# Performance work log

Measured on AMD Instinct MI355X. Metric: run time of the kernel, lower is better.

Reference implementation:

```python
import jax, jax.numpy as jnp
import numpy as np

D_MODEL = 512
D_FFN = 4 * D_MODEL
EPS = 1e-5


def layer_norm(x, gamma, beta):
    mu = jnp.mean(x, axis=-1, keepdims=True)
    var = jnp.mean(jnp.square(x - mu), axis=-1, keepdims=True)
    return (x - mu) * jax.lax.rsqrt(var + EPS) * gamma + beta


def setup_inputs() -> dict:
    key = jax.random.key(0)
    ks = jax.random.split(key, 12)
    B, S, D, F = 4, 2048, D_MODEL, D_FFN
    s = 1.0 / np.sqrt(D)
    inp = {
        "q": jax.random.normal(ks[0], (B, S, D), jnp.float32),
        "k": jax.random.normal(ks[1], (B, S, D), jnp.float32),
        "v": jax.random.normal(ks[2], (B, S, D), jnp.float32),
        "x": jax.random.normal(ks[3], (B, S, D), jnp.float32),
        "Wq": jax.random.normal(ks[4], (D, D), jnp.float32) * s,
        "bq": jnp.zeros((D,), jnp.float32),
        "Wk": jax.random.normal(ks[5], (D, D), jnp.float32) * s,
        "bk": jnp.zeros((D,), jnp.float32),
        "Wv": jax.random.normal(ks[6], (D, D), jnp.float32) * s,
        "bv": jnp.zeros((D,), jnp.float32),
        "g1": jnp.ones((D,), jnp.float32),
        "be1": jnp.zeros((D,), jnp.float32),
        "W1": jax.random.normal(ks[7], (D, F), jnp.float32) * s,
        "b1": jnp.zeros((F,), jnp.float32),
        "W2": jax.random.normal(ks[8], (F, D), jnp.float32) * (1.0 / np.sqrt(F)),
        "b2": jnp.zeros((D,), jnp.float32),
        "g2": jnp.ones((D,), jnp.float32),
        "be2": jnp.zeros((D,), jnp.float32),
    }
    return inp


def reference(q, k, v, x, Wq, bq, Wk, bk, Wv, bv, g1, be1, W1, b1, W2, b2, g2, be2):
    # QKV projections: [B,S,D] @ [D,D]
    Q = jnp.einsum("bsd,de->bse", q, Wq) + bq
    K = jnp.einsum("bsd,de->bse", k, Wk) + bk
    V = jnp.einsum("bsd,de->bse", v, Wv) + bv
    d_k = Q.shape[-1]
    # scaled dot-product attention, full [B,S,S] scores as in the original
    scores = jnp.einsum("bqd,bkd->bqk", Q, K) / jnp.sqrt(jnp.float32(d_k))
    probs = jax.nn.softmax(scores, axis=-1)
    attn = jnp.einsum("bqk,bkd->bqd", probs, V)
    # residual + LayerNorm
    h = layer_norm(attn + x, g1, be1)
    # position-wise FFN
    f = jnp.maximum(jnp.einsum("bsd,df->bsf", h, W1) + b1, 0.0)
    f = jnp.einsum("bsf,fd->bsd", f, W2) + b2
    # residual + LayerNorm
    return layer_norm(f + h, g2, be2)
```

## Files before the change

### kernel.cpp

```cpp
#include <hip/hip_runtime.h>


typedef __attribute__((ext_vector_type(8))) short short8;
typedef __attribute__((ext_vector_type(4))) float f32x4;

__device__ __forceinline__ unsigned short f2bf(float f) {
    unsigned int u = __float_as_uint(f);
    unsigned int r = (u + 0x7FFFu + ((u >> 16) & 1u)) >> 16;
    return (unsigned short)r;
}

__device__ __forceinline__ void gload_lds16(const void* g, void* l) {
    __builtin_amdgcn_global_load_lds(
        (const __attribute__((address_space(1))) void*)g,
        (__attribute__((address_space(3))) void*)l, 16, 0, 0);
}

__global__ __launch_bounds__(256) void cast_f32_bf16(
    const float* __restrict__ in, unsigned short* __restrict__ out, long n4) {
    long i = (long)blockIdx.x * blockDim.x + threadIdx.x;
    if (i < n4) {
        float4 v = ((const float4*)in)[i];
        ushort4 o;
        o.x = f2bf(v.x); o.y = f2bf(v.y); o.z = f2bf(v.z); o.w = f2bf(v.w);
        ((ushort4*)out)[i] = o;
    }
}

__global__ __launch_bounds__(256) void concat3(
    const float* __restrict__ a, const float* __restrict__ b,
    const float* __restrict__ c, float* __restrict__ o, int n) {
    int i = blockIdx.x * blockDim.x + threadIdx.x;
    if (i < n) o[i] = a[i];
    else if (i < 2 * n) o[i] = b[i - n];
    else if (i < 3 * n) o[i] = c[i - 2 * n];
}

__global__ __launch_bounds__(256) void transpose_cast_f32_bf16(
    const float* __restrict__ in, unsigned short* __restrict__ out, int R, int C) {
    __shared__ float t[32][33];
    int c0 = blockIdx.x * 32, r0 = blockIdx.y * 32;
    int x = threadIdx.x;
    for (int i = threadIdx.y; i < 32; i += 8)
        t[i][x] = in[(long)(r0 + i) * C + c0 + x];
    __syncthreads();
    for (int i = threadIdx.y; i < 32; i += 8)
        out[(long)(c0 + i) * R + r0 + x] = f2bf(t[x][i]);
}

__global__ __launch_bounds__(256) void transpose_bf16(
    const unsigned short* __restrict__ in, unsigned short* __restrict__ out,
    int R, int C, int inLd, long inBatch, long outBatch) {
    __shared__ unsigned short t[32][33];
    long z = blockIdx.z;
    in += z * inBatch; out += z * outBatch;
    int c0 = blockIdx.x * 32, r0 = blockIdx.y * 32;
    int x = threadIdx.x;
    for (int i = threadIdx.y; i < 32; i += 8)
        t[i][x] = in[(long)(r0 + i) * inLd + c0 + x];
    __syncthreads();
    for (int i = threadIdx.y; i < 32; i += 8)
        out[(long)(c0 + i) * R + r0 + x] = t[x][i];
}

template<int BIAS, int RELU, int OUT_BF16>
__global__ __launch_bounds__(256, 2) void gemm_nt(
    const unsigned short* __restrict__ A, const unsigned short* __restrict__ BT,
    const float* __restrict__ bias, void* __restrict__ C,
    int K, int lda, int ldb, int ldc,
    long aBatch, long bBatch, long cBatch,
    long aKOff, long bKOff, long cKOff, int zDiv,
    long aGroup, float scale) {
    __shared__ __align__(16) unsigned short As[2][4096];
    __shared__ __align__(16) unsigned short Bs[2][4096];
    const int tid  = threadIdx.x;
    const int wave = tid >> 6;
    const int lane = tid & 63;
    const int z = blockIdx.z;
    const int b = z / zDiv;
    const int kc = z - b * zDiv;
    const int row0 = blockIdx.y * 128;
    const int col0 = blockIdx.x * 128;
    A  += (long)b * aBatch + (long)kc * aKOff + (long)(col0 >> 9) * aGroup;
    BT += (long)b * bBatch + (long)kc * bKOff;
    const long cOff = (long)b * cBatch + (long)kc * cKOff;
    const int wr = (wave >> 1) * 64;
    const int wc = (wave & 1) * 64;

    f32x4 acc[4][4] = {};

    const int fs = ((tid >> 2) & 3) ^ ((tid >> 4) & 3);
    const unsigned short* Ag = A  + (long)(row0 + (tid >> 2)) * lda + (((tid & 3) ^ fs) << 3);
    const unsigned short* Bg = BT + (long)(col0 + (tid >> 2)) * ldb + (((tid & 3) ^ fs) << 3);
    const int sBase = wave * 512;

    const int lr  = lane & 15;
    const int fr  = (lr & 3) ^ ((lr >> 2) & 3);
    const int kq8 = (((lane >> 4) ^ fr) << 3);
    const int nk = K >> 5;

    #pragma unroll
    for (int c = 0; c < 2; ++c) {
        gload_lds16(Ag + (long)c * 64 * lda, &As[0][sBase + c * 2048]);
        gload_lds16(Bg + (long)c * 64 * ldb, &Bs[0][sBase + c * 2048]);
    }
    __syncthreads();

    for (int t = 0; t < nk; ++t) {
        const int cur = t & 1;
        if (t + 1 < nk) {
            const int k0 = (t + 1) << 5;
            #pragma unroll
            for (int c = 0; c < 2; ++c) {
                gload_lds16(Ag + (long)c * 64 * lda + k0, &As[cur ^ 1][sBase + c * 2048]);
                gload_lds16(Bg + (long)c * 64 * ldb + k0, &Bs[cur ^ 1][sBase + c * 2048]);
            }
        }
        short8 af[4], bf[4];
        #pragma unroll
        for (int m = 0; m < 4; ++m)
            af[m] = *(const short8*)&As[cur][(wr + m * 16 + lr) * 32 + kq8];
        #pragma unroll
        for (int n = 0; n < 4; ++n)
            bf[n] = *(const short8*)&Bs[cur][(wc + n * 16 + lr) * 32 + kq8];
        #pragma unroll
        for (int m = 0; m < 4; ++m)
            #pragma unroll
            for (int n = 0; n < 4; ++n)
                acc[m][n] = __builtin_amdgcn_mfma_f32_16x16x32_bf16(
                    af[m], bf[n], acc[m][n], 0, 0, 0);
        __syncthreads();
    }

    const int orow = row0 + wr + (lane >> 4) * 4;
    const int ocol = col0 + wc + lr;
    #pragma unroll
    for (int n = 0; n < 4; ++n) {
        const int cc = ocol + n * 16;
        float bv = 0.0f;
        if (BIAS) bv = bias[cc];
        #pragma unroll
        for (int m = 0; m < 4; ++m) {
            #pragma unroll
            for (int j = 0; j < 4; ++j) {
                float v = acc[m][n][j] * scale + bv;
                if (RELU) v = fmaxf(v, 0.0f);
                long off = cOff + (long)(orow + m * 16 + j) * ldc + cc;
                if (OUT_BF16) ((unsigned short*)C)[off] = f2bf(v);
                else          ((float*)C)[off] = v;
            }
        }
    }
}

__global__ __launch_bounds__(256) void softmax_rows(
    const float* __restrict__ S, unsigned short* __restrict__ P) {
    long row = blockIdx.x;
    const float4* src = (const float4*)(S + row * 2048);
    int tid = threadIdx.x;
    int wave = tid >> 6, lane = tid & 63;
    float4 a = src[tid], b = src[tid + 256];
    float e[8] = { a.x, a.y, a.z, a.w, b.x, b.y, b.z, b.w };
    float m = e[0];
    #pragma unroll
    for (int i = 1; i < 8; ++i) m = fmaxf(m, e[i]);
    #pragma unroll
    for (int o = 32; o > 0; o >>= 1) m = fmaxf(m, __shfl_xor(m, o));
    __shared__ float redm[4], reds[4];
    if (lane == 0) redm[wave] = m;
    __syncthreads();
    m = fmaxf(fmaxf(redm[0], redm[1]), fmaxf(redm[2], redm[3]));
    float s = 0.0f;
    #pragma unroll
    for (int i = 0; i < 8; ++i) { e[i] = __expf(e[i] - m); s += e[i]; }
    #pragma unroll
    for (int o = 32; o > 0; o >>= 1) s += __shfl_xor(s, o);
    if (lane == 0) reds[wave] = s;
    __syncthreads();
    s = reds[0] + reds[1] + reds[2] + reds[3];
    float inv = 1.0f / s;
    ushort4 o0, o1;
    o0.x = f2bf(e[0] * inv); o0.y = f2bf(e[1] * inv);
    o0.z = f2bf(e[2] * inv); o0.w = f2bf(e[3] * inv);
    o1.x = f2bf(e[4] * inv); o1.y = f2bf(e[5] * inv);
    o1.z = f2bf(e[6] * inv); o1.w = f2bf(e[7] * inv);
    ushort4* dst = (ushort4*)(P + row * 2048);
    dst[tid] = o0;
    dst[tid + 256] = o1;
}

template<int NPART, int BIASF, int DUAL>
__global__ __launch_bounds__(128) void ln_kernel(
    const float* __restrict__ A0, long partOff, const float* __restrict__ R,
    const float* __restrict__ bias,
    const float* __restrict__ g, const float* __restrict__ be,
    float* __restrict__ out, unsigned short* __restrict__ outbf) {
    long row = blockIdx.x;
    int tid = threadIdx.x;
    int wave = tid >> 6, lane = tid & 63;
    float4 va = ((const float4*)(A0 + row * 512))[tid];
    float4 vr = ((const float4*)(R + row * 512))[tid];
    float4 v;
    v.x = va.x + vr.x; v.y = va.y + vr.y; v.z = va.z + vr.z; v.w = va.w + vr.w;
    if (NPART == 2) {
        float4 vp = ((const float4*)(A0 + partOff + row * 512))[tid];
        v.x += vp.x; v.y += vp.y; v.z += vp.z; v.w += vp.w;
    }
    if (BIASF) {
        float4 vb = ((const float4*)bias)[tid];
        v.x += vb.x; v.y += vb.y; v.z += vb.z; v.w += vb.w;
    }
    float s  = v.x + v.y + v.z + v.w;
    float s2 = v.x * v.x + v.y * v.y + v.z * v.z + v.w * v.w;
    #pragma unroll
    for (int o = 32; o > 0; o >>= 1) { s += __shfl_xor(s, o); s2 += __shfl_xor(s2, o); }
    __shared__ float r1[2], r2[2];
    if (lane == 0) { r1[wave] = s; r2[wave] = s2; }
    __syncthreads();
    s = r1[0] + r1[1]; s2 = r2[0] + r2[1];
    float mu = s * (1.0f / 512.0f);
    float var = s2 * (1.0f / 512.0f) - mu * mu;
    float rs = rsqrtf(var + 1e-5f);
    float4 gg = ((const float4*)g)[tid];
    float4 bb = ((const float4*)be)[tid];
    float4 y;
    y.x = (v.x - mu) * rs * gg.x + bb.x;
    y.y = (v.y - mu) * rs * gg.y + bb.y;
    y.z = (v.z - mu) * rs * gg.z + bb.z;
    y.w = (v.w - mu) * rs * gg.w + bb.w;
    ((float4*)(out + row * 512))[tid] = y;
    if (DUAL) {
        ushort4 o;
        o.x = f2bf(y.x); o.y = f2bf(y.y); o.z = f2bf(y.z); o.w = f2bf(y.w);
        ((ushort4*)(outbf + row * 512))[tid] = o;
    }
}

extern "C" void kernel_launch(void* const* d_in, const int* in_sizes, int n_in,
                              void* d_out, int out_size, void* d_ws, size_t ws_size,
                              hipStream_t stream) {
    const float* q   = (const float*)d_in[0];
    const float* k   = (const float*)d_in[1];
    const float* v   = (const float*)d_in[2];
    const float* x   = (const float*)d_in[3];
    const float* Wq  = (const float*)d_in[4];
    const float* bq  = (const float*)d_in[5];
    const float* Wk  = (const float*)d_in[6];
    const float* bk  = (const float*)d_in[7];
    const float* Wv  = (const float*)d_in[8];
    const float* bv  = (const float*)d_in[9];
    const float* g1  = (const float*)d_in[10];
    const float* be1 = (const float*)d_in[11];
    const float* W1  = (const float*)d_in[12];
    const float* b1  = (const float*)d_in[13];
    const float* W2  = (const float*)d_in[14];
    const float* b2  = (const float*)d_in[15];
    const float* g2  = (const float*)d_in[16];
    const float* be2 = (const float*)d_in[17];
    float* out = (float*)d_out;

    const int B = 4, S = 2048, D = 512, F = 2048;
    const long BS = (long)B * S;
    const long SD = (long)S * D;
    const long SS = (long)S * S;
    const int N3 = 3 * D;

    char* ws = (char*)d_ws;
    size_t off = 0;
    auto alloc = [&](size_t bytes) -> void* {
        void* p = ws + off;
        off += (bytes + 255) & ~(size_t)255;
        return p;
    };
    unsigned short* WqkvT = (unsigned short*)alloc((size_t)N3 * D * 2);
    unsigned short* W1T   = (unsigned short*)alloc((size_t)D * F * 2);
    unsigned short* W2T   = (unsigned short*)alloc((size_t)F * D * 2);
    float* bqkv           = (float*)alloc((size_t)N3 * 4);
    unsigned short* qkv_in = (unsigned short*)alloc(3 * BS * D * 2);
    unsigned short* VT = qkv_in;
    unsigned short* QKV = (unsigned short*)alloc(BS * (size_t)N3 * 2);
    float* h_f32 = (float*)QKV;
    unsigned short* h_bf = (unsigned short*)((char*)QKV + BS * D * 4);
    float* Sc = (float*)alloc((size_t)B * SS * 4);
    float* attnP = Sc;
    float* f2P   = Sc;
    unsigned short* Pb = (unsigned short*)alloc((size_t)B * SS * 2);
    unsigned short* f_bf = Pb;

    const float scale = 0.04419417382415922f;

    {
        long n4 = BS * D / 4;
        int blocks = (int)((n4 + 255) / 256);
        cast_f32_bf16<<<blocks, 256, 0, stream>>>(q, qkv_in, n4);
        cast_f32_bf16<<<blocks, 256, 0, stream>>>(k, qkv_in + BS * D, n4);
        cast_f32_bf16<<<blocks, 256, 0, stream>>>(v, qkv_in + 2 * BS * D, n4);
    }
    transpose_cast_f32_bf16<<<dim3(D/32, D/32), dim3(32, 8), 0, stream>>>(Wq, WqkvT, D, D);
    transpose_cast_f32_bf16<<<dim3(D/32, D/32), dim3(32, 8), 0, stream>>>(Wk, WqkvT + (size_t)D * D, D, D);
    transpose_cast_f32_bf16<<<dim3(D/32, D/32), dim3(32, 8), 0, stream>>>(Wv, WqkvT + 2 * (size_t)D * D, D, D);
    transpose_cast_f32_bf16<<<dim3(F/32, D/32), dim3(32, 8), 0, stream>>>(W1, W1T, D, F);
    transpose_cast_f32_bf16<<<dim3(D/32, F/32), dim3(32, 8), 0, stream>>>(W2, W2T, F, D);
    concat3<<<(3 * D + 255) / 256, 256, 0, stream>>>(bq, bk, bv, bqkv, D);
    gemm_nt<1,0,1><<<dim3(N3/128, BS/128, 1), 256, 0, stream>>>(
        qkv_in, WqkvT, bqkv, QKV, D, D, D, N3,
        0, 0, 0, 0, 0, 0, 1, BS * D, 1.0f);
    transpose_bf16<<<dim3(D/32, S/32, B), dim3(32, 8), 0, stream>>>(
        QKV + 2 * D, VT, S, D, N3, (long)S * N3, SD);
    gemm_nt<0,0,0><<<dim3(S/128, S/128, B), 256, 0, stream>>>(
        QKV, QKV + D, nullptr, Sc, D, N3, N3, S,
        (long)S * N3, (long)S * N3, SS, 0, 0, 0, 1, 0, scale);
    softmax_rows<<<(int)BS, 256, 0, stream>>>(Sc, Pb);
    gemm_nt<0,0,0><<<dim3(D/128, S/128, 2 * B), 256, 0, stream>>>(
        Pb, VT, nullptr, attnP, S / 2, S, S, D,
        SS, SD, SD, S / 2, S / 2, BS * D, 2, 0, 1.0f);
    ln_kernel<2,0,1><<<(int)BS, 128, 0, stream>>>(attnP, BS * D, x, nullptr, g1, be1, h_f32, h_bf);
    gemm_nt<1,1,1><<<dim3(F/128, BS/128, 1), 256, 0, stream>>>(
        h_bf, W1T, b1, f_bf, D, D, D, F,
        0, 0, 0, 0, 0, 0, 1, 0, 1.0f);
    gemm_nt<0,0,0><<<dim3(D/128, BS/128, 2), 256, 0, stream>>>(
        f_bf, W2T, nullptr, f2P, F / 2, F, F, D,
        0, 0, 0, F / 2, F / 2, BS * D, 2, 0, 1.0f);
    ln_kernel<2,1,0><<<(int)BS, 128, 0, stream>>>(f2P, BS * D, h_f32, b2, g2, be2, out, nullptr);
}
```

Before: 354.7 us.

## Replace 128x128 GEMM with 256x256 eight-wave pipelined kernel and 4-way split-K

Swaps the 128x128, 4-wave bf16 MFMA GEMM for a 256x256, 8-wave kernel with a K-tile of 64 and a swizzled LDS layout. Global-to-LDS loads are staged in quarters interleaved with MFMA groups, using explicit vmcnt/lgkmcnt waits, raw barriers and setprio. The PV and FFN2 GEMMs move from 2-way to 4-way split-K to keep grid sizes near the CU count, and the LayerNorm kernels now sum four partial slabs. This aims for more reuse per loaded tile and better overlap of loads with compute, at the cost of 64KB of LDS per block, more partial-sum traffic, and fragile hand-written wait counts.

```diff
diff --git a/kernel.cpp b/kernel.cpp
--- a/kernel.cpp
+++ b/kernel.cpp
@@ -3,6 +3,10 @@
 
 typedef __attribute__((ext_vector_type(8))) short short8;
 typedef __attribute__((ext_vector_type(4))) float f32x4;
+
+#define BARRIER()   asm volatile("s_barrier" ::: "memory")
+#define WAITVM(N)   asm volatile("s_waitcnt vmcnt(" #N ")" ::: "memory")
+#define WAITLGKM0() asm volatile("s_waitcnt lgkmcnt(0)" ::: "memory")
 
 __device__ __forceinline__ unsigned short f2bf(float f) {
     unsigned int u = __float_as_uint(f);
@@ -64,88 +68,135 @@
 }
 
 template<int BIAS, int RELU, int OUT_BF16>
-__global__ __launch_bounds__(256, 2) void gemm_nt(
+__global__ __launch_bounds__(512, 2) void gemm256(
     const unsigned short* __restrict__ A, const unsigned short* __restrict__ BT,
     const float* __restrict__ bias, void* __restrict__ C,
     int K, int lda, int ldb, int ldc,
     long aBatch, long bBatch, long cBatch,
     long aKOff, long bKOff, long cKOff, int zDiv,
     long aGroup, float scale) {
-    __shared__ __align__(16) unsigned short As[2][4096];
-    __shared__ __align__(16) unsigned short Bs[2][4096];
+    __shared__ __align__(16) unsigned short As[2][16384];
+    __shared__ __align__(16) unsigned short Bs[2][16384];
     const int tid  = threadIdx.x;
     const int wave = tid >> 6;
     const int lane = tid & 63;
+    const int wm = wave >> 2;
+    const int wn = wave & 3;
     const int z = blockIdx.z;
     const int b = z / zDiv;
     const int kc = z - b * zDiv;
-    const int row0 = blockIdx.y * 128;
-    const int col0 = blockIdx.x * 128;
-    A  += (long)b * aBatch + (long)kc * aKOff + (long)(col0 >> 9) * aGroup;
-    BT += (long)b * bBatch + (long)kc * bKOff;
+    const int row0 = blockIdx.y * 256;
+    const int col0 = blockIdx.x * 256;
+    A  += (long)b * aBatch + (long)kc * aKOff + (long)(col0 >> 9) * aGroup
+        + (long)row0 * lda;
+    BT += (long)b * bBatch + (long)kc * bKOff + (long)col0 * ldb;
     const long cOff = (long)b * cBatch + (long)kc * cKOff;
-    const int wr = (wave >> 1) * 64;
-    const int wc = (wave & 1) * 64;
-
-    f32x4 acc[4][4] = {};
-
-    const int fs = ((tid >> 2) & 3) ^ ((tid >> 4) & 3);
-    const unsigned short* Ag = A  + (long)(row0 + (tid >> 2)) * lda + (((tid & 3) ^ fs) << 3);
-    const unsigned short* Bg = BT + (long)(col0 + (tid >> 2)) * ldb + (((tid & 3) ^ fs) << 3);
-    const int sBase = wave * 512;
-
-    const int lr  = lane & 15;
-    const int fr  = (lr & 3) ^ ((lr >> 2) & 3);
-    const int kq8 = (((lane >> 4) ^ fr) << 3);
-    const int nk = K >> 5;
-
-    #pragma unroll
-    for (int c = 0; c < 2; ++c) {
-        gload_lds16(Ag + (long)c * 64 * lda, &As[0][sBase + c * 2048]);
-        gload_lds16(Bg + (long)c * 64 * ldb, &Bs[0][sBase + c * 2048]);
-    }
-    __syncthreads();
-
-    for (int t = 0; t < nk; ++t) {
-        const int cur = t & 1;
-        if (t + 1 < nk) {
-            const int k0 = (t + 1) << 5;
+
+    f32x4 acc[8][4] = {};
+
+    const int sr = tid >> 3;
+    const int sc = (tid & 7) ^ (sr & 7);
+    const long aSrcOff = (long)sr * lda + sc * 8;
+    const long bSrcOff = (long)sr * ldb + sc * 8;
+    const int ldst = wave << 9;
+    const int nt = K >> 6;
+
+    const int rA = lane & 15, l4 = lane >> 4;
+    const int cp0 = ((l4)     ^ (rA & 7)) << 3;
+    const int cp1 = ((4 + l4) ^ (rA & 7)) << 3;
+
+#define STAGE_A(t, a) gload_lds16(A  + (long)(t) * 64 + (long)(a) * 64 * lda + aSrcOff, \
+                                  &As[(t) & 1][(a) * 4096 + ldst])
+#define STAGE_B(t, a) gload_lds16(BT + (long)(t) * 64 + (long)(a) * 64 * ldb + bSrcOff, \
+                                  &Bs[(t) & 1][(a) * 4096 + ldst])
+
+    STAGE_B(0, 0); STAGE_B(0, 1); STAGE_B(0, 2); STAGE_B(0, 3);
+    STAGE_A(0, 0); STAGE_A(0, 1); STAGE_A(0, 2); STAGE_A(0, 3);
+    STAGE_B(1, 0); STAGE_B(1, 1); STAGE_B(1, 2); STAGE_B(1, 3);
+    STAGE_A(1, 0); STAGE_A(1, 2);
+    WAITVM(6);
+    BARRIER();
+
+    for (int t = 0; t < nt; ++t) {
+        const int buf = t & 1;
+        short8 bfr[4][2];
+        short8 afr[2][2];
+        #pragma unroll
+        for (int fn = 0; fn < 4; ++fn) {
+            const int rb = (wn * 64 + fn * 16 + rA) * 64;
+            bfr[fn][0] = *(const short8*)&Bs[buf][rb + cp0];
+            bfr[fn][1] = *(const short8*)&Bs[buf][rb + cp1];
+        }
+        #pragma unroll
+        for (int i = 0; i < 2; ++i) {
+            const int ra = (wm * 128 + i * 16 + rA) * 64;
+            afr[i][0] = *(const short8*)&As[buf][ra + cp0];
+            afr[i][1] = *(const short8*)&As[buf][ra + cp1];
+        }
+        if (t + 1 < nt) { STAGE_A(t + 1, 1); STAGE_A(t + 1, 3); }
+        BARRIER();
+        WAITLGKM0();
+        __builtin_amdgcn_sched_barrier(0);
+        __builtin_amdgcn_s_setprio(1);
+        #pragma unroll
+        for (int ks = 0; ks < 2; ++ks)
             #pragma unroll
-            for (int c = 0; c < 2; ++c) {
-                gload_lds16(Ag + (long)c * 64 * lda + k0, &As[cur ^ 1][sBase + c * 2048]);
-                gload_lds16(Bg + (long)c * 64 * ldb + k0, &Bs[cur ^ 1][sBase + c * 2048]);
+            for (int i = 0; i < 2; ++i)
+                #pragma unroll
+                for (int fn = 0; fn < 4; ++fn)
+                    acc[i][fn] = __builtin_amdgcn_mfma_f32_16x16x32_bf16(
+                        afr[i][ks], bfr[fn][ks], acc[i][fn], 0, 0, 0);
+        __builtin_amdgcn_s_setprio(0);
+        BARRIER();
+        #pragma unroll
+        for (int q = 1; q < 4; ++q) {
+            #pragma unroll
+            for (int i = 0; i < 2; ++i) {
+                const int ra = (wm * 128 + (2 * q + i) * 16 + rA) * 64;
+                afr[i][0] = *(const short8*)&As[buf][ra + cp0];
+                afr[i][1] = *(const short8*)&As[buf][ra + cp1];
             }
+            if (q == 1 && t + 2 < nt) { STAGE_B(t + 2, 0); STAGE_B(t + 2, 1); }
+            if (q == 2 && t + 2 < nt) { STAGE_B(t + 2, 2); STAGE_B(t + 2, 3); }
+            if (q == 3 && t + 2 < nt) { STAGE_A(t + 2, 0); STAGE_A(t + 2, 2); }
+            BARRIER();
+            WAITLGKM0();
+            __builtin_amdgcn_sched_barrier(0);
+            __builtin_amdgcn_s_setprio(1);
+            #pragma unroll
+            for (int ks = 0; ks < 2; ++ks)
+                #pragma unroll
+                for (int i = 0; i < 2; ++i)
+                    #pragma unroll
+                    for (int fn = 0; fn < 4; ++fn)
+                        acc[2 * q + i][fn] = __builtin_amdgcn_mfma_f32_16x16x32_bf16(
+                            afr[i][ks], bfr[fn][ks], acc[2 * q + i][fn], 0, 0, 0);
+            __builtin_amdgcn_s_setprio(0);
+            if (q == 1 && t == nt - 1) { WAITVM(0); }
+            if (q == 3) {
+                if (t + 2 < nt)       { WAITVM(6); }
+                else if (t + 2 == nt) { WAITVM(2); }
+            }
+            BARRIER();
         }
-        short8 af[4], bf[4];
-        #pragma unroll
-        for (int m = 0; m < 4; ++m)
-            af[m] = *(const short8*)&As[cur][(wr + m * 16 + lr) * 32 + kq8];
-        #pragma unroll
-        for (int n = 0; n < 4; ++n)
-            bf[n] = *(const short8*)&Bs[cur][(wc + n * 16 + lr) * 32 + kq8];
-        #pragma unroll
-        for (int m = 0; m < 4; ++m)
-            #pragma unroll
-            for (int n = 0; n < 4; ++n)
-                acc[m][n] = __builtin_amdgcn_mfma_f32_16x16x32_bf16(
-                    af[m], bf[n], acc[m][n], 0, 0, 0);
-        __syncthreads();
-    }
-
-    const int orow = row0 + wr + (lane >> 4) * 4;
-    const int ocol = col0 + wc + lr;
-    #pragma unroll
-    for (int n = 0; n < 4; ++n) {
-        const int cc = ocol + n * 16;
+    }
+#undef STAGE_A
+#undef STAGE_B
+
+    const int orow = row0 + wm * 128 + l4 * 4;
+    const int ocol = col0 + wn * 64 + rA;
+    #pragma unroll
+    for (int fn = 0; fn < 4; ++fn) {
+        const int cc = ocol + fn * 16;
         float bv = 0.0f;
         if (BIAS) bv = bias[cc];
         #pragma unroll
-        for (int m = 0; m < 4; ++m) {
+        for (int fm = 0; fm < 8; ++fm) {
             #pragma unroll
             for (int j = 0; j < 4; ++j) {
-                float v = acc[m][n][j] * scale + bv;
+                float v = acc[fm][fn][j] * scale + bv;
                 if (RELU) v = fmaxf(v, 0.0f);
-                long off = cOff + (long)(orow + m * 16 + j) * ldc + cc;
+                long off = cOff + (long)(orow + fm * 16 + j) * ldc + cc;
                 if (OUT_BF16) ((unsigned short*)C)[off] = f2bf(v);
                 else          ((float*)C)[off] = v;
             }
@@ -198,12 +249,10 @@
     long row = blockIdx.x;
     int tid = threadIdx.x;
     int wave = tid >> 6, lane = tid & 63;
-    float4 va = ((const float4*)(A0 + row * 512))[tid];
-    float4 vr = ((const float4*)(R + row * 512))[tid];
-    float4 v;
-    v.x = va.x + vr.x; v.y = va.y + vr.y; v.z = va.z + vr.z; v.w = va.w + vr.w;
-    if (NPART == 2) {
-        float4 vp = ((const float4*)(A0 + partOff + row * 512))[tid];
+    float4 v = ((const float4*)(R + row * 512))[tid];
+    #pragma unroll
+    for (int p = 0; p < NPART; ++p) {
+        float4 vp = ((const float4*)(A0 + p * partOff + row * 512))[tid];
         v.x += vp.x; v.y += vp.y; v.z += vp.z; v.w += vp.w;
     }
     if (BIASF) {
@@ -302,24 +351,24 @@
     transpose_cast_f32_bf16<<<dim3(F/32, D/32), dim3(32, 8), 0, stream>>>(W1, W1T, D, F);
     transpose_cast_f32_bf16<<<dim3(D/32, F/32), dim3(32, 8), 0, stream>>>(W2, W2T, F, D);
     concat3<<<(3 * D + 255) / 256, 256, 0, stream>>>(bq, bk, bv, bqkv, D);
-    gemm_nt<1,0,1><<<dim3(N3/128, BS/128, 1), 256, 0, stream>>>(
+    gemm256<1,0,1><<<dim3(N3/256, 32, 1), 512, 0, stream>>>(
         qkv_in, WqkvT, bqkv, QKV, D, D, D, N3,
         0, 0, 0, 0, 0, 0, 1, BS * D, 1.0f);
     transpose_bf16<<<dim3(D/32, S/32, B), dim3(32, 8), 0, stream>>>(
         QKV + 2 * D, VT, S, D, N3, (long)S * N3, SD);
-    gemm_nt<0,0,0><<<dim3(S/128, S/128, B), 256, 0, stream>>>(
+    gemm256<0,0,0><<<dim3(S/256, S/256, B), 512, 0, stream>>>(
         QKV, QKV + D, nullptr, Sc, D, N3, N3, S,
         (long)S * N3, (long)S * N3, SS, 0, 0, 0, 1, 0, scale);
     softmax_rows<<<(int)BS, 256, 0, stream>>>(Sc, Pb);
-    gemm_nt<0,0,0><<<dim3(D/128, S/128, 2 * B), 256, 0, stream>>>(
-        Pb, VT, nullptr, attnP, S / 2, S, S, D,
-        SS, SD, SD, S / 2, S / 2, BS * D, 2, 0, 1.0f);
-    ln_kernel<2,0,1><<<(int)BS, 128, 0, stream>>>(attnP, BS * D, x, nullptr, g1, be1, h_f32, h_bf);
-    gemm_nt<1,1,1><<<dim3(F/128, BS/128, 1), 256, 0, stream>>>(
+    gemm256<0,0,0><<<dim3(D/256, S/256, 4 * B), 512, 0, stream>>>(
+        Pb, VT, nullptr, attnP, S / 4, S, S, D,
+        SS, SD, SD, S / 4, S / 4, BS * D, 4, 0, 1.0f);
+    ln_kernel<4,0,1><<<(int)BS, 128, 0, stream>>>(attnP, BS * D, x, nullptr, g1, be1, h_f32, h_bf);
+    gemm256<1,1,1><<<dim3(F/256, 32, 1), 512, 0, stream>>>(
         h_bf, W1T, b1, f_bf, D, D, D, F,
         0, 0, 0, 0, 0, 0, 1, 0, 1.0f);
-    gemm_nt<0,0,0><<<dim3(D/128, BS/128, 2), 256, 0, stream>>>(
-        f_bf, W2T, nullptr, f2P, F / 2, F, F, D,
-        0, 0, 0, F / 2, F / 2, BS * D, 2, 0, 1.0f);
-    ln_kernel<2,1,0><<<(int)BS, 128, 0, stream>>>(f2P, BS * D, h_f32, b2, g2, be2, out, nullptr);
-}
+    gemm256<0,0,0><<<dim3(D/256, 32, 4), 512, 0, stream>>>(
+        f_bf, W2T, nullptr, f2P, F / 4, F, F, D,
+        0, 0, 0, F / 4, F / 4, BS * D, 4, 0, 1.0f);
+    ln_kernel<4,1,0><<<(int)BS, 128, 0, stream>>>(f2P, BS * D, h_f32, b2, g2, be2, out, nullptr);
+}
```

After: 364.9 us. +2.9%, slower.
